# Kernel optimization log

Hardware: AMD Instinct MI355X
Metric: run time of the kernel (lower is better)

## Reference

```python
import jax, jax.numpy as jnp
import numpy as np

NUM_GROUPS = 32
EPS = 1e-6


def setup_inputs() -> dict:
    key = jax.random.key(0)
    ks = jax.random.split(key, 11)
    B, C, L = 4, 256, 4096
    s = 1.0 / np.sqrt(C)
    return {
        "x": jax.random.normal(ks[0], (B, C, L), dtype=jnp.float32),
        "gn_w": jnp.ones((C,), dtype=jnp.float32),
        "gn_b": jnp.zeros((C,), dtype=jnp.float32),
        "qw": jax.random.normal(ks[1], (C, C), dtype=jnp.float32) * s,
        "qb": jnp.zeros((C,), dtype=jnp.float32),
        "kw": jax.random.normal(ks[2], (C, C), dtype=jnp.float32) * s,
        "kb": jnp.zeros((C,), dtype=jnp.float32),
        "vw": jax.random.normal(ks[3], (C, C), dtype=jnp.float32) * s,
        "vb": jnp.zeros((C,), dtype=jnp.float32),
        "pw": jax.random.normal(ks[4], (C, C), dtype=jnp.float32) * s,
        "pb": jnp.zeros((C,), dtype=jnp.float32),
    }


def group_norm(x, w, b):
    # x: [B, C, L]; normalize over (C//G, L) within each of G=32 groups
    B, C, L = x.shape
    xg = x.reshape(B, NUM_GROUPS, (C // NUM_GROUPS) * L)
    mean = jnp.mean(xg, axis=2, keepdims=True)
    var = jnp.var(xg, axis=2, keepdims=True)
    xn = ((xg - mean) * jax.lax.rsqrt(var + EPS)).reshape(B, C, L)
    return xn * w[None, :, None] + b[None, :, None]


def conv1x1(x, w, b):
    # 1x1 Conv1d == channel matmul: [O,C] x [B,C,L] -> [B,O,L]
    return jnp.einsum('oc,bcl->bol', w, x) + b[None, :, None]


def reference(x, gn_w, gn_b, qw, qb, kw, kb, vw, vb, pw, pb):
    B, C, L = x.shape
    scale = C ** (-0.5)
    xn = group_norm(x, gn_w, gn_b)
    q = conv1x1(xn, qw, qb)
    k = conv1x1(xn, kw, kb)
    v = conv1x1(xn, vw, vb)
    attn = jnp.einsum('bci,bcj->bij', q, k) * scale  # [B, L, L]
    attn = jax.nn.softmax(attn, axis=2)
    out = jnp.einsum('bij,bcj->bci', attn, v)  # [B, C, L]
    out = conv1x1(out, pw, pb)
    return x + out
```

## Files before the change

### kernel.cpp

```cpp
#include <hip/hip_runtime.h>
#include <hip/hip_bf16.h>

#define B_ 4
#define C_ 256
#define L_ 4096
#define G_ 32
#define KVS_ 4

typedef __attribute__((ext_vector_type(8))) short bf16x8;
typedef __attribute__((ext_vector_type(4))) float f32x4;
typedef __attribute__((ext_vector_type(16))) float f32x16;
typedef __attribute__((ext_vector_type(4))) unsigned short us4;
typedef __attribute__((ext_vector_type(8))) unsigned short us8;
typedef __attribute__((ext_vector_type(4))) unsigned int u32x4;

__device__ __forceinline__ unsigned short f2bf(float f) {
  unsigned u = __builtin_bit_cast(unsigned, f);
  u += 0x7fffu + ((u >> 16) & 1u);
  return (unsigned short)(u >> 16);
}
__device__ __forceinline__ float bf2f(unsigned short s) {
  return __builtin_bit_cast(float, (unsigned)s << 16);
}

__device__ __forceinline__ void async_copy16(const void* g, void* l) {
  __builtin_amdgcn_global_load_lds((const __attribute__((address_space(1))) void*)g,
                                   (__attribute__((address_space(3))) void*)l, 16, 0, 0);
}

__global__ void wcvt_kernel(const float* __restrict__ qw, const float* __restrict__ kw,
                            const float* __restrict__ vw, const float* __restrict__ pw,
                            unsigned short* __restrict__ dst) {
  int m = blockIdx.x >> 6;
  const float* src = (m == 0) ? qw : ((m == 1) ? kw : ((m == 2) ? vw : pw));
  int i = ((blockIdx.x & 63) * 256 + threadIdx.x) * 4;
  float4 v = *(const float4*)(src + i);
  us4 o;
  o[0] = f2bf(v.x); o[1] = f2bf(v.y); o[2] = f2bf(v.z); o[3] = f2bf(v.w);
  *(us4*)(dst + m * C_ * C_ + i) = o;
}

__global__ __launch_bounds__(256) void gn_kernel(const float* __restrict__ x,
                                                 const float* __restrict__ gw,
                                                 const float* __restrict__ gb,
                                                 unsigned short* __restrict__ xn_t) {
  int bg = blockIdx.x;
  int b = bg >> 5, g = bg & 31;
  const float* xp = x + (size_t)bg * 8 * L_;
  float s = 0.f, ss = 0.f;
  for (int i = threadIdx.x * 4; i < 8 * L_; i += 1024) {
    float4 v = *(const float4*)(xp + i);
    s += v.x + v.y + v.z + v.w;
    ss += v.x * v.x + v.y * v.y + v.z * v.z + v.w * v.w;
  }
#pragma unroll
  for (int m = 1; m < 64; m <<= 1) { s += __shfl_xor(s, m); ss += __shfl_xor(ss, m); }
  __shared__ float red[8];
  int w = threadIdx.x >> 6;
  if ((threadIdx.x & 63) == 0) { red[w] = s; red[4 + w] = ss; }
  __syncthreads();
  s = red[0] + red[1] + red[2] + red[3];
  ss = red[4] + red[5] + red[6] + red[7];
  const float inv_n = 1.f / (8.f * L_);
  float mean = s * inv_n;
  float rstd = rsqrtf(ss * inv_n - mean * mean + 1e-6f);

  float sw[8], sb[8];
#pragma unroll
  for (int j = 0; j < 8; ++j) {
    int c = g * 8 + j;
    sw[j] = gw[c] * rstd;
    sb[j] = gb[c] - mean * sw[j];
  }
#pragma unroll 1
  for (int lc = 0; lc < 4; ++lc) {
    int l = lc * 1024 + threadIdx.x * 4;
    float res[4][8];
#pragma unroll
    for (int j = 0; j < 8; ++j) {
      float4 v = *(const float4*)(x + ((size_t)b * C_ + g * 8 + j) * L_ + l);
      res[0][j] = v.x * sw[j] + sb[j]; res[1][j] = v.y * sw[j] + sb[j];
      res[2][j] = v.z * sw[j] + sb[j]; res[3][j] = v.w * sw[j] + sb[j];
    }
#pragma unroll
    for (int i = 0; i < 4; ++i) {
      us8 o;
#pragma unroll
      for (int j = 0; j < 8; ++j) o[j] = f2bf(res[i][j]);
      *(us8*)(xn_t + ((size_t)b * L_ + l + i) * C_ + g * 8) = o;
    }
  }
}

__global__ __launch_bounds__(256) void qkv_gemm_kernel(
    const unsigned short* __restrict__ wq, const unsigned short* __restrict__ wk,
    const unsigned short* __restrict__ wv, const float* __restrict__ qbias,
    const float* __restrict__ kbias, const float* __restrict__ vbias,
    const unsigned short* __restrict__ xn, unsigned short* __restrict__ qt,
    unsigned short* __restrict__ kt, unsigned short* __restrict__ vt) {
  int id = blockIdx.x;
  int nt = id & 63, mt = (id >> 6) & 3, b = (id >> 8) & 3;
  int lane = threadIdx.x & 63, wid = threadIdx.x >> 6;
  int ln = lane & 15, lq = lane >> 4;
  int m0 = mt * 64 + wid * 16;
  int n0 = nt * 64;
  const unsigned short* xb = xn + (size_t)b * L_ * C_;
  bf16x8 aq[8], ak[8], av[8];
  const unsigned short* arow = wq + (m0 + ln) * C_ + lq * 8;
#pragma unroll
  for (int ks = 0; ks < 8; ++ks) aq[ks] = *(const bf16x8*)(arow + ks * 32);
  arow = wk + (m0 + ln) * C_ + lq * 8;
#pragma unroll
  for (int ks = 0; ks < 8; ++ks) ak[ks] = *(const bf16x8*)(arow + ks * 32);
  arow = wv + (m0 + ln) * C_ + lq * 8;
#pragma unroll
  for (int ks = 0; ks < 8; ++ks) av[ks] = *(const bf16x8*)(arow + ks * 32);

  int o0 = m0 + lq * 4;
  float bq[4], bk[4], bv[4];
#pragma unroll
  for (int r = 0; r < 4; ++r) { bq[r] = qbias[o0 + r]; bk[r] = kbias[o0 + r]; bv[r] = vbias[o0 + r]; }
  unsigned short* qd = qt + (size_t)b * L_ * C_;
  unsigned short* kd = kt + (size_t)b * L_ * C_;
  unsigned short* vd = vt + (size_t)b * C_ * L_;
  const float QSCALE = 0.0625f * 1.44269504f;

#pragma unroll
  for (int t = 0; t < 4; ++t) {
    f32x4 cq = {0.f, 0.f, 0.f, 0.f}, ck = cq, cv = cq;
    const unsigned short* brow = xb + (size_t)(n0 + 16 * t + ln) * C_ + lq * 8;
#pragma unroll
    for (int ks = 0; ks < 8; ++ks) {
      bf16x8 bf = *(const bf16x8*)(brow + ks * 32);
      cq = __builtin_amdgcn_mfma_f32_16x16x32_bf16(aq[ks], bf, cq, 0, 0, 0);
      ck = __builtin_amdgcn_mfma_f32_16x16x32_bf16(ak[ks], bf, ck, 0, 0, 0);
      cv = __builtin_amdgcn_mfma_f32_16x16x32_bf16(av[ks], bf, cv, 0, 0, 0);
    }
    int l = n0 + 16 * t + ln;
    us4 pk;
#pragma unroll
    for (int r = 0; r < 4; ++r) pk[r] = f2bf((cq[r] + bq[r]) * QSCALE);
    *(us4*)(qd + (size_t)l * C_ + o0) = pk;
#pragma unroll
    for (int r = 0; r < 4; ++r) pk[r] = f2bf(ck[r] + bk[r]);
    *(us4*)(kd + (size_t)l * C_ + o0) = pk;
#pragma unroll
    for (int r = 0; r < 4; ++r) vd[(size_t)(o0 + r) * L_ + l] = f2bf(cv[r] + bv[r]);
  }
}

__global__ __launch_bounds__(512) void attn_kernel(
    const unsigned short* __restrict__ qt, const unsigned short* __restrict__ kt,
    const unsigned short* __restrict__ vt, unsigned short* __restrict__ po,
    float2* __restrict__ ml) {
  __shared__ __attribute__((aligned(16))) char Kl[2][16384];
  __shared__ __attribute__((aligned(16))) char Vl[2][16384];

  int idx = (blockIdx.x & 7) * 32 + (blockIdx.x >> 3);
  int g = idx >> 4;
  int qtile = idx & 15;
  int b = g >> 2, s = g & 3;
  int jbase = s * (L_ / KVS_);
  const int NIT = (L_ / KVS_) / 32;

  int tid = threadIdx.x;
  int lane = tid & 63, wid = tid >> 6;
  int lq = lane & 31;
  int lk = lane >> 5;
  int q0 = qtile * 256 + wid * 32;

  const unsigned short* qb_ = qt + (size_t)b * L_ * C_;
  const unsigned short* kb_ = kt + (size_t)b * L_ * C_;
  const unsigned short* vb_ = vt + (size_t)b * C_ * L_;

  auto stage = [&](int j0, int bs) {
#pragma unroll
    for (int r = 0; r < 2; ++r) {
      int addr = r * 8192 + tid * 16;
      int row = addr >> 9, colb = addr & 511;
      async_copy16((const char*)kb_ + (size_t)(j0 + row) * 512 + (colb ^ ((row & 7) << 4)),
                   Kl[bs] + addr);
    }
#pragma unroll
    for (int r = 0; r < 2; ++r) {
      int addr = r * 8192 + tid * 16;
      int c = addr >> 6, colb = addr & 63;
      async_copy16((const char*)vb_ + (size_t)c * (L_ * 2) + (size_t)j0 * 2 +
                       (colb ^ (((c >> 1) & 3) << 4)),
                   Vl[bs] + addr);
    }
  };

  bf16x8 qf[16];
  const unsigned short* qrow = qb_ + (size_t)(q0 + lq) * C_ + lk * 8;
#pragma unroll
  for (int kc = 0; kc < 16; ++kc) qf[kc] = *(const bf16x8*)(qrow + kc * 16);

  stage(jbase, 0);
  stage(jbase + 32, 1);

  f32x16 oacc[8];
#pragma unroll
  for (int ct = 0; ct < 8; ++ct)
#pragma unroll
    for (int i = 0; i < 16; ++i) oacc[ct][i] = 0.f;

  float m_run = -3e38f, l_run = 0.f;
  const int kswz = (lq & 7) << 4;
  const int vswz = ((lq >> 1) & 3) << 4;

#pragma unroll 1
  for (int jt = 0; jt < NIT; ++jt) {
    const char* Kb = Kl[jt & 1];
    const char* Vb = Vl[jt & 1];

    asm volatile("s_waitcnt vmcnt(8)" ::: "memory");
    __builtin_amdgcn_sched_barrier(0);
    __builtin_amdgcn_s_barrier();
    __builtin_amdgcn_sched_barrier(0);

    f32x16 sa, sb;
#pragma unroll
    for (int i = 0; i < 16; ++i) { sa[i] = 0.f; sb[i] = 0.f; }
    __builtin_amdgcn_s_setprio(1);
#pragma unroll
    for (int kc = 0; kc < 16; kc += 2) {
      bf16x8 kf0 = *(const bf16x8*)(Kb + lq * 512 + ((kc * 32 + lk * 16) ^ kswz));
      sa = __builtin_amdgcn_mfma_f32_32x32x16_bf16(kf0, qf[kc], sa, 0, 0, 0);
      bf16x8 kf1 = *(const bf16x8*)(Kb + lq * 512 + (((kc + 1) * 32 + lk * 16) ^ kswz));
      sb = __builtin_amdgcn_mfma_f32_32x32x16_bf16(kf1, qf[kc + 1], sb, 0, 0, 0);
    }
    __builtin_amdgcn_s_setprio(0);
    f32x16 sacc = sa + sb;

    float pm = sacc[0];
#pragma unroll
    for (int i = 1; i < 16; ++i) pm = fmaxf(pm, sacc[i]);
    pm = fmaxf(pm, __shfl_xor(pm, 32));
    if (__any(pm > m_run + 8.0f)) {
      float mn = fmaxf(m_run, pm);
      float al = exp2f(m_run - mn);
      l_run *= al;
#pragma unroll
      for (int ct = 0; ct < 8; ++ct)
#pragma unroll
        for (int i = 0; i < 16; ++i) oacc[ct][i] *= al;
      m_run = mn;
    }
    float p[16];
    float ls = 0.f;
#pragma unroll
    for (int i = 0; i < 16; ++i) {
      p[i] = exp2f(sacc[i] - m_run);
      ls += p[i];
    }
    ls += __shfl_xor(ls, 32);
    l_run += ls;

    unsigned w[8];
#pragma unroll
    for (int i = 0; i < 8; ++i)
      asm("v_cvt_pk_bf16_f32 %0, %1, %2" : "=v"(w[i]) : "v"(p[2 * i]), "v"(p[2 * i + 1]));
    asm volatile("v_permlane32_swap_b32 %0, %1" : "+v"(w[0]), "+v"(w[2]));
    asm volatile("v_permlane32_swap_b32 %0, %1" : "+v"(w[1]), "+v"(w[3]));
    asm volatile("v_permlane32_swap_b32 %0, %1" : "+v"(w[4]), "+v"(w[6]));
    asm volatile("v_permlane32_swap_b32 %0, %1" : "+v"(w[5]), "+v"(w[7]));
    u32x4 t1 = {w[0], w[1], w[2], w[3]};
    u32x4 t2 = {w[4], w[5], w[6], w[7]};
    bf16x8 pb1 = __builtin_bit_cast(bf16x8, t1);
    bf16x8 pb2 = __builtin_bit_cast(bf16x8, t2);

    __builtin_amdgcn_s_setprio(1);
#pragma unroll
    for (int ct = 0; ct < 8; ++ct) {
      int vr = ct * 32 + lq;
      bf16x8 av0 = *(const bf16x8*)(Vb + vr * 64 + ((lk * 16) ^ vswz));
      oacc[ct] = __builtin_amdgcn_mfma_f32_32x32x16_bf16(av0, pb1, oacc[ct], 0, 0, 0);
      bf16x8 av1 = *(const bf16x8*)(Vb + vr * 64 + ((32 + lk * 16) ^ vswz));
      oacc[ct] = __builtin_amdgcn_mfma_f32_32x32x16_bf16(av1, pb2, oacc[ct], 0, 0, 0);
    }
    __builtin_amdgcn_s_setprio(0);

    __builtin_amdgcn_sched_barrier(0);
    __builtin_amdgcn_s_barrier();
    __builtin_amdgcn_sched_barrier(0);
    stage(jbase + ((jt + 2) & (NIT - 1)) * 32, jt & 1);
  }

  asm volatile("s_waitcnt vmcnt(0)" ::: "memory");

  unsigned short* pob = po + ((size_t)g * L_ + q0 + lq) * C_;
#pragma unroll
  for (int ct = 0; ct < 8; ++ct) {
#pragma unroll
    for (int e = 0; e < 4; ++e) {
      us4 pk;
#pragma unroll
      for (int r = 0; r < 4; ++r) pk[r] = f2bf(oacc[ct][4 * e + r]);
      *(us4*)(pob + ct * 32 + 8 * e + 4 * lk) = pk;
    }
  }
  if (lane < 32)
    ml[(size_t)g * L_ + q0 + lq] = make_float2(m_run, l_run);
}

__global__ void combine_kernel(const unsigned short* __restrict__ po,
                               const float2* __restrict__ ml,
                               unsigned short* __restrict__ ot) {
  int tid = threadIdx.x;
  int row = blockIdx.x * 4 + (tid >> 6);
  int b = row >> 12;
  int l = row & (L_ - 1);
  int lane = tid & 63;
  float2 mv[KVS_];
  float M = -3e38f;
#pragma unroll
  for (int s = 0; s < KVS_; ++s) {
    mv[s] = ml[(size_t)(b * KVS_ + s) * L_ + l];
    M = fmaxf(M, mv[s].x);
  }
  float acc[4] = {0.f, 0.f, 0.f, 0.f};
  float denom = 0.f;
#pragma unroll
  for (int s = 0; s < KVS_; ++s) {
    float w = exp2f(mv[s].x - M);
    denom += w * mv[s].y;
    us4 o = *(const us4*)(po + ((size_t)(b * KVS_ + s) * L_ + l) * C_ + lane * 4);
#pragma unroll
    for (int j = 0; j < 4; ++j) acc[j] += w * bf2f(o[j]);
  }
  float inv = 1.f / denom;
  us4 o;
#pragma unroll
  for (int j = 0; j < 4; ++j) o[j] = f2bf(acc[j] * inv);
  *(us4*)(ot + (size_t)row * C_ + lane * 4) = o;
}

__global__ __launch_bounds__(256) void proj_kernel(
    const unsigned short* __restrict__ wp, const float* __restrict__ pbias,
    const unsigned short* __restrict__ ot, const float* __restrict__ x,
    float* __restrict__ out) {
  int id = blockIdx.x;
  int nt = id & 63, mt = (id >> 6) & 3, b = id >> 8;
  int lane = threadIdx.x & 63, wid = threadIdx.x >> 6;
  int ln = lane & 15, lq = lane >> 4;
  int m0 = mt * 64 + wid * 16;
  int n0 = nt * 64;
  const unsigned short* ob = ot + (size_t)b * L_ * C_;
  bf16x8 a[8];
  const unsigned short* arow = wp + (m0 + ln) * C_ + lq * 8;
#pragma unroll
  for (int ks = 0; ks < 8; ++ks) a[ks] = *(const bf16x8*)(arow + ks * 32);
  f32x4 acc[4];
#pragma unroll
  for (int t = 0; t < 4; ++t) {
    f32x4 c = {0.f, 0.f, 0.f, 0.f};
    const unsigned short* brow = ob + (size_t)(n0 + 16 * t + ln) * C_ + lq * 8;
#pragma unroll
    for (int ks = 0; ks < 8; ++ks) {
      bf16x8 bf = *(const bf16x8*)(brow + ks * 32);
      c = __builtin_amdgcn_mfma_f32_16x16x32_bf16(a[ks], bf, c, 0, 0, 0);
    }
    acc[t] = c;
  }
  int o0 = m0 + lq * 4;
#pragma unroll
  for (int r = 0; r < 4; ++r) {
    float bvr = pbias[o0 + r];
    const float* xrow = x + ((size_t)b * C_ + o0 + r) * L_;
    float* orow = out + ((size_t)b * C_ + o0 + r) * L_;
#pragma unroll
    for (int t = 0; t < 4; ++t) {
      int l = n0 + 16 * t + ln;
      orow[l] = xrow[l] + acc[t][r] + bvr;
    }
  }
}

extern "C" void kernel_launch(void* const* d_in, const int* in_sizes, int n_in,
                              void* d_out, int out_size, void* d_ws, size_t ws_size,
                              hipStream_t stream) {
  const float* x   = (const float*)d_in[0];
  const float* gnw = (const float*)d_in[1];
  const float* gnb = (const float*)d_in[2];
  const float* qw  = (const float*)d_in[3];
  const float* qb  = (const float*)d_in[4];
  const float* kw  = (const float*)d_in[5];
  const float* kb  = (const float*)d_in[6];
  const float* vw  = (const float*)d_in[7];
  const float* vb  = (const float*)d_in[8];
  const float* pw  = (const float*)d_in[9];
  const float* pb  = (const float*)d_in[10];
  float* out = (float*)d_out;

  unsigned short* ws = (unsigned short*)d_ws;
  const size_t SZ = (size_t)B_ * L_ * C_;
  unsigned short* xn_t = ws;
  unsigned short* qt   = xn_t + SZ;
  unsigned short* kt   = qt + SZ;
  unsigned short* vt   = kt + SZ;
  unsigned short* ot   = vt + SZ;
  unsigned short* wb   = ot + SZ;
  unsigned short* po   = wb + 4 * C_ * C_;
  float2* ml = (float2*)(po + (size_t)KVS_ * SZ);

  wcvt_kernel<<<256, 256, 0, stream>>>(qw, kw, vw, pw, wb);
  gn_kernel<<<B_ * G_, 256, 0, stream>>>(x, gnw, gnb, xn_t);
  qkv_gemm_kernel<<<1024, 256, 0, stream>>>(wb, wb + C_ * C_, wb + 2 * C_ * C_,
                                            qb, kb, vb, xn_t, qt, kt, vt);
  attn_kernel<<<256, 512, 0, stream>>>(qt, kt, vt, po, ml);
  combine_kernel<<<B_ * L_ / 4, 256, 0, stream>>>(po, ml, ot);
  proj_kernel<<<1024, 256, 0, stream>>>(wb + 3 * C_ * C_, pb, ot, x, out);
}
```

Baseline: 212.6 us.

## Template KV split count, use 8 splits when workspace allows, single-buffer V

Makes the attention kernel's KV split factor a template parameter and picks 8 splits when the workspace is large enough, so 512 blocks launch instead of 256 and more CUs are filled. V shared memory drops from double to single buffering, which shrinks LDS so more blocks fit per CU. V for the next tile is now staged right after the end-of-iteration barrier, and the wait count drops to vmcnt(2). In exchange the combine kernel reads twice as many partial outputs, its loop over splits is now a runtime loop, and V loads have less time to overlap with compute.

```diff
diff --git a/kernel.cpp b/kernel.cpp
--- a/kernel.cpp
+++ b/kernel.cpp
@@ -5,7 +5,6 @@
 #define C_ 256
 #define L_ 4096
 #define G_ 32
-#define KVS_ 4
 
 typedef __attribute__((ext_vector_type(8))) short bf16x8;
 typedef __attribute__((ext_vector_type(4))) float f32x4;
@@ -149,19 +148,23 @@
   }
 }
 
+template <int KVS>
 __global__ __launch_bounds__(512) void attn_kernel(
     const unsigned short* __restrict__ qt, const unsigned short* __restrict__ kt,
     const unsigned short* __restrict__ vt, unsigned short* __restrict__ po,
     float2* __restrict__ ml) {
   __shared__ __attribute__((aligned(16))) char Kl[2][16384];
-  __shared__ __attribute__((aligned(16))) char Vl[2][16384];
-
-  int idx = (blockIdx.x & 7) * 32 + (blockIdx.x >> 3);
+  __shared__ __attribute__((aligned(16))) char Vl[16384];
+
+  constexpr int KSH = (KVS == 8) ? 3 : 2;
+  constexpr int NIT = (L_ / KVS) / 32;
+  const int NBLK = B_ * KVS * 16;
+
+  int idx = (blockIdx.x & 7) * (NBLK >> 3) + (blockIdx.x >> 3);
   int g = idx >> 4;
   int qtile = idx & 15;
-  int b = g >> 2, s = g & 3;
-  int jbase = s * (L_ / KVS_);
-  const int NIT = (L_ / KVS_) / 32;
+  int b = g >> KSH, s = g & (KVS - 1);
+  int jbase = s * (L_ / KVS);
 
   int tid = threadIdx.x;
   int lane = tid & 63, wid = tid >> 6;
@@ -173,21 +176,23 @@
   const unsigned short* kb_ = kt + (size_t)b * L_ * C_;
   const unsigned short* vb_ = vt + (size_t)b * C_ * L_;
 
-  auto stage = [&](int j0, int bs) {
+  auto stageK = [&](int j0, char* Kb) {
 #pragma unroll
     for (int r = 0; r < 2; ++r) {
       int addr = r * 8192 + tid * 16;
       int row = addr >> 9, colb = addr & 511;
       async_copy16((const char*)kb_ + (size_t)(j0 + row) * 512 + (colb ^ ((row & 7) << 4)),
-                   Kl[bs] + addr);
-    }
+                   Kb + addr);
+    }
+  };
+  auto stageV = [&](int j0) {
 #pragma unroll
     for (int r = 0; r < 2; ++r) {
       int addr = r * 8192 + tid * 16;
       int c = addr >> 6, colb = addr & 63;
       async_copy16((const char*)vb_ + (size_t)c * (L_ * 2) + (size_t)j0 * 2 +
                        (colb ^ (((c >> 1) & 3) << 4)),
-                   Vl[bs] + addr);
+                   Vl + addr);
     }
   };
 
@@ -196,8 +201,9 @@
 #pragma unroll
   for (int kc = 0; kc < 16; ++kc) qf[kc] = *(const bf16x8*)(qrow + kc * 16);
 
-  stage(jbase, 0);
-  stage(jbase + 32, 1);
+  stageK(jbase, Kl[0]);
+  stageV(jbase);
+  stageK(jbase + 32, Kl[1]);
 
   f32x16 oacc[8];
 #pragma unroll
@@ -212,9 +218,8 @@
 #pragma unroll 1
   for (int jt = 0; jt < NIT; ++jt) {
     const char* Kb = Kl[jt & 1];
-    const char* Vb = Vl[jt & 1];
-
-    asm volatile("s_waitcnt vmcnt(8)" ::: "memory");
+
+    asm volatile("s_waitcnt vmcnt(2)" ::: "memory");
     __builtin_amdgcn_sched_barrier(0);
     __builtin_amdgcn_s_barrier();
     __builtin_amdgcn_sched_barrier(0);
@@ -274,9 +279,9 @@
 #pragma unroll
     for (int ct = 0; ct < 8; ++ct) {
       int vr = ct * 32 + lq;
-      bf16x8 av0 = *(const bf16x8*)(Vb + vr * 64 + ((lk * 16) ^ vswz));
+      bf16x8 av0 = *(const bf16x8*)(Vl + vr * 64 + ((lk * 16) ^ vswz));
       oacc[ct] = __builtin_amdgcn_mfma_f32_32x32x16_bf16(av0, pb1, oacc[ct], 0, 0, 0);
-      bf16x8 av1 = *(const bf16x8*)(Vb + vr * 64 + ((32 + lk * 16) ^ vswz));
+      bf16x8 av1 = *(const bf16x8*)(Vl + vr * 64 + ((32 + lk * 16) ^ vswz));
       oacc[ct] = __builtin_amdgcn_mfma_f32_32x32x16_bf16(av1, pb2, oacc[ct], 0, 0, 0);
     }
     __builtin_amdgcn_s_setprio(0);
@@ -284,7 +289,8 @@
     __builtin_amdgcn_sched_barrier(0);
     __builtin_amdgcn_s_barrier();
     __builtin_amdgcn_sched_barrier(0);
-    stage(jbase + ((jt + 2) & (NIT - 1)) * 32, jt & 1);
+    stageV(jbase + ((jt + 1) & (NIT - 1)) * 32);
+    stageK(jbase + ((jt + 2) & (NIT - 1)) * 32, Kl[jt & 1]);
   }
 
   asm volatile("s_waitcnt vmcnt(0)" ::: "memory");
@@ -306,26 +312,24 @@
 
 __global__ void combine_kernel(const unsigned short* __restrict__ po,
                                const float2* __restrict__ ml,
-                               unsigned short* __restrict__ ot) {
+                               unsigned short* __restrict__ ot, int kvs) {
   int tid = threadIdx.x;
   int row = blockIdx.x * 4 + (tid >> 6);
   int b = row >> 12;
   int l = row & (L_ - 1);
   int lane = tid & 63;
-  float2 mv[KVS_];
+  float2 mv[8];
   float M = -3e38f;
-#pragma unroll
-  for (int s = 0; s < KVS_; ++s) {
-    mv[s] = ml[(size_t)(b * KVS_ + s) * L_ + l];
+  for (int s = 0; s < kvs; ++s) {
+    mv[s] = ml[(size_t)(b * kvs + s) * L_ + l];
     M = fmaxf(M, mv[s].x);
   }
   float acc[4] = {0.f, 0.f, 0.f, 0.f};
   float denom = 0.f;
-#pragma unroll
-  for (int s = 0; s < KVS_; ++s) {
+  for (int s = 0; s < kvs; ++s) {
     float w = exp2f(mv[s].x - M);
     denom += w * mv[s].y;
-    us4 o = *(const us4*)(po + ((size_t)(b * KVS_ + s) * L_ + l) * C_ + lane * 4);
+    us4 o = *(const us4*)(po + ((size_t)(b * kvs + s) * L_ + l) * C_ + lane * 4);
 #pragma unroll
     for (int j = 0; j < 4; ++j) acc[j] += w * bf2f(o[j]);
   }
@@ -395,6 +399,11 @@
 
   unsigned short* ws = (unsigned short*)d_ws;
   const size_t SZ = (size_t)B_ * L_ * C_;
+
+  size_t need8 = (5 * SZ + 4 * C_ * C_ + 8 * SZ) * sizeof(unsigned short) +
+                 (size_t)B_ * 8 * L_ * sizeof(float2) + 256;
+  int KVS = (ws_size >= need8) ? 8 : 4;
+
   unsigned short* xn_t = ws;
   unsigned short* qt   = xn_t + SZ;
   unsigned short* kt   = qt + SZ;
@@ -402,13 +411,16 @@
   unsigned short* ot   = vt + SZ;
   unsigned short* wb   = ot + SZ;
   unsigned short* po   = wb + 4 * C_ * C_;
-  float2* ml = (float2*)(po + (size_t)KVS_ * SZ);
+  float2* ml = (float2*)(po + (size_t)KVS * SZ);
 
   wcvt_kernel<<<256, 256, 0, stream>>>(qw, kw, vw, pw, wb);
   gn_kernel<<<B_ * G_, 256, 0, stream>>>(x, gnw, gnb, xn_t);
   qkv_gemm_kernel<<<1024, 256, 0, stream>>>(wb, wb + C_ * C_, wb + 2 * C_ * C_,
                                             qb, kb, vb, xn_t, qt, kt, vt);
-  attn_kernel<<<256, 512, 0, stream>>>(qt, kt, vt, po, ml);
-  combine_kernel<<<B_ * L_ / 4, 256, 0, stream>>>(po, ml, ot);
+  if (KVS == 8)
+    attn_kernel<8><<<B_ * 8 * 16, 512, 0, stream>>>(qt, kt, vt, po, ml);
+  else
+    attn_kernel<4><<<B_ * 4 * 16, 512, 0, stream>>>(qt, kt, vt, po, ml);
+  combine_kernel<<<B_ * L_ / 4, 256, 0, stream>>>(po, ml, ot, KVS);
   proj_kernel<<<1024, 256, 0, stream>>>(wb + 3 * C_ * C_, pb, ot, x, out);
 }
```

Result: slower. 277.6 us (+30.5%).
